# Performance work log

Measured on AMD Instinct MI355X. Metric: run time of the kernel, lower is better.

Reference implementation:

```python
import jax, jax.numpy as jnp
import numpy as np

B, T, I, H, NL, HORIZON, NQ = 256, 512, 64, 512, 2, 30, 3
MEDIAN_IDX = 1  # quantiles.index(0.5)


def _lstm_cell(xt, h, c, Wih, Whh, b):
    # PyTorch gate order: i, f, g, o
    g = xt @ Wih.T + h @ Whh.T + b
    i, f, gg, o = jnp.split(g, 4, axis=-1)
    c_new = jax.nn.sigmoid(f) * c + jax.nn.sigmoid(i) * jnp.tanh(gg)
    h_new = jax.nn.sigmoid(o) * jnp.tanh(c_new)
    return h_new, c_new


def _run_lstm_layer(xs, Wih, Whh, b):
    # xs: [T, B, in]; zero initial state (torch default)
    batch = xs.shape[1]
    hidden = Whh.shape[1]
    h0 = jnp.zeros((batch, hidden), xs.dtype)

    def step(carry, xt):
        h, c = carry
        h, c = _lstm_cell(xt, h, c, Wih, Whh, b)
        return (h, c), h

    (hT, cT), hs = jax.lax.scan(step, (h0, h0), xs)
    return hs, hT, cT


def setup_inputs() -> dict:
    key = jax.random.key(0)
    ks = jax.random.split(key, 24)
    k = 1.0 / np.sqrt(H)

    def u(kk, shape):
        return jax.random.uniform(kk, shape, jnp.float32, -k, k)

    inp = {
        "x": jax.random.normal(ks[0], (B, T, I), jnp.float32),
        # encoder layer 0 (input I) and layer 1 (input H)
        "enc_Wih0": u(ks[1], (4 * H, I)),
        "enc_Whh0": u(ks[2], (4 * H, H)),
        "enc_bih0": u(ks[3], (4 * H,)),
        "enc_bhh0": u(ks[4], (4 * H,)),
        "enc_Wih1": u(ks[5], (4 * H, H)),
        "enc_Whh1": u(ks[6], (4 * H, H)),
        "enc_bih1": u(ks[7], (4 * H,)),
        "enc_bhh1": u(ks[8], (4 * H,)),
        # decoder layer 0 (input H+1) and layer 1 (input H)
        "dec_Wih0": u(ks[9], (4 * H, H + 1)),
        "dec_Whh0": u(ks[10], (4 * H, H)),
        "dec_bih0": u(ks[11], (4 * H,)),
        "dec_bhh0": u(ks[12], (4 * H,)),
        "dec_Wih1": u(ks[13], (4 * H, H)),
        "dec_Whh1": u(ks[14], (4 * H, H)),
        "dec_bih1": u(ks[15], (4 * H,)),
        "dec_bhh1": u(ks[16], (4 * H,)),
        # attention: W [H,H] (no bias), V [H] (Linear(H,1) weight)
        "attn_W": u(ks[17], (H, H)),
        "attn_v": u(ks[18], (H,)),
        # output projection [NQ, H] + bias
        "out_W": u(ks[19], (NQ, H)),
        "out_b": u(ks[20], (NQ,)),
    }
    return inp


def reference(x, enc_Wih0, enc_Whh0, enc_bih0, enc_bhh0,
              enc_Wih1, enc_Whh1, enc_bih1, enc_bhh1,
              dec_Wih0, dec_Whh0, dec_bih0, dec_bhh0,
              dec_Wih1, dec_Whh1, dec_bih1, dec_bhh1,
              attn_W, attn_v, out_W, out_b):
    # ---- encoder: 2-layer LSTM over time (eval mode: no dropout) ----
    xs = jnp.transpose(x, (1, 0, 2))  # [T, B, I]
    hs0, _, _ = _run_lstm_layer(xs, enc_Wih0, enc_Whh0, enc_bih0 + enc_bhh0)
    hs1, h_last, c_last = _run_lstm_layer(hs0, enc_Wih1, enc_Whh1, enc_bih1 + enc_bhh1)
    encoder_outputs = jnp.transpose(hs1, (1, 0, 2))  # [B, T, H]

    # precompute W(encoder_outputs) once (same math as per-step recompute)
    enc_proj = jnp.einsum('bth,gh->btg', encoder_outputs, attn_W)  # [B, T, H]

    b_dec0 = dec_bih0 + dec_bhh0
    b_dec1 = dec_bih1 + dec_bhh1

    dec_input0 = x[:, -1, 0:1]  # [B, 1]

    def step(carry, _):
        h, c, inp = carry
        # Bahdanau attention
        dec_proj = h @ attn_W.T  # [B, H]
        energies = jnp.einsum('bth,h->bt', jnp.tanh(enc_proj + dec_proj[:, None, :]), attn_v)
        attn = jax.nn.softmax(energies, axis=1)  # [B, T]
        ctx = jnp.einsum('bt,bth->bh', attn, encoder_outputs)  # [B, H]
        # decoder LSTM, 1 timestep; both layers restart from the SAME (h, c)
        # (the module repeats the last layer's state across layers each step)
        x0 = jnp.concatenate([inp, ctx], axis=1)  # [B, H+1]
        h0, c0 = _lstm_cell(x0, h, c, dec_Wih0, dec_Whh0, b_dec0)
        h1, c1 = _lstm_cell(h0, h, c, dec_Wih1, dec_Whh1, b_dec1)
        out = h1 @ out_W.T + out_b  # [B, NQ]
        new_inp = out[:, MEDIAN_IDX:MEDIAN_IDX + 1]  # feed back median quantile
        return (h1, c1, new_inp), out

    _, preds = jax.lax.scan(step, (h_last, c_last, dec_input0), None, length=HORIZON)
    return jnp.transpose(preds, (1, 0, 2))  # [B, HORIZON, NQ]
```

## Files before the change

### kernel.cpp

```cpp
#include <hip/hip_runtime.h>


typedef _Float16 half_t;
typedef __attribute__((ext_vector_type(8)))  _Float16 f16x8;
typedef __attribute__((ext_vector_type(16))) float    f32x16;

#define MFMA(a,b,c) __builtin_amdgcn_mfma_f32_32x32x16_f16((a),(b),(c),0,0,0)
#define CBAR()      asm volatile("" ::: "memory")
#define AUXC 17

template<int N> __device__ __forceinline__ void waitvm() {
  asm volatile("s_waitcnt vmcnt(%0)" :: "n"(N) : "memory");
}

__device__ __forceinline__ float fsig(float x)  { return 1.0f / (1.0f + __expf(-x)); }
__device__ __forceinline__ float ftanh(float x) { return 1.0f - 2.0f / (1.0f + __expf(2.0f * x)); }

union FU { float f; unsigned u; };
union HU { _Float16 h; unsigned short u; };
__device__ __forceinline__ float ldfa(const float* p) {
  unsigned v = __hip_atomic_load((const unsigned*)p, __ATOMIC_RELAXED, __HIP_MEMORY_SCOPE_AGENT);
  FU c; c.u = v; return c.f;
}
__device__ __forceinline__ void stfa(float* p, float v) {
  FU c; c.f = v;
  __hip_atomic_store((unsigned*)p, c.u, __ATOMIC_RELAXED, __HIP_MEMORY_SCOPE_AGENT);
}
__device__ __forceinline__ void stha(half_t* p, float v) {
  HU c; c.h = (half_t)v;
  __hip_atomic_store((unsigned short*)p, c.u, __ATOMIC_RELAXED, __HIP_MEMORY_SCOPE_AGENT);
}
__device__ __forceinline__ void st64(float* p, float a, float b) {
  FU x, y; x.f = a; y.f = b;
  unsigned long long v = (unsigned long long)x.u | ((unsigned long long)y.u << 32);
  __hip_atomic_store((unsigned long long*)p, v, __ATOMIC_RELAXED, __HIP_MEMORY_SCOPE_AGENT);
}
__device__ __forceinline__ void ld64(const float* p, float& a, float& b) {
  unsigned long long v = __hip_atomic_load((const unsigned long long*)p, __ATOMIC_RELAXED, __HIP_MEMORY_SCOPE_AGENT);
  FU x, y; x.u = (unsigned)v; y.u = (unsigned)(v >> 32); a = x.f; b = y.f;
}

static constexpr size_t O_X16 = 0;
static constexpr size_t O_WL0 = O_X16 + (size_t)512*256*128*2;
static constexpr size_t O_WL1 = O_WL0 + (size_t)2048*640*2;
static constexpr size_t O_WP1 = O_WL1 + (size_t)2048*1024*2;
static constexpr size_t O_WD0 = O_WP1 + (size_t)4672*512*2;
static constexpr size_t O_WD1 = O_WD0 + (size_t)2048*512*2;
static constexpr size_t O_BL0 = O_WD1 + (size_t)2048*512*2;
static constexpr size_t O_BL1 = O_BL0 + 8192;
static constexpr size_t O_BD0 = O_BL1 + 8192;
static constexpr size_t O_BD1 = O_BD0 + 8192;
static constexpr size_t O_W0C = O_BD1 + 8192;
static constexpr size_t O_H0B = O_W0C + 8192;
static constexpr size_t O_H1B = O_H0B + (size_t)2*256*512*2;
static constexpr size_t O_HD1 = O_H1B + (size_t)2*256*512*2;
static constexpr size_t O_H0D = O_HD1 + (size_t)256*512*2;
static constexpr size_t O_CTX = O_H0D + (size_t)256*512*2;
static constexpr size_t O_C0  = O_CTX + (size_t)256*512*2;
static constexpr size_t O_C1  = O_C0  + (size_t)256*512*4;
static constexpr size_t O_INP = O_C1  + (size_t)256*512*4;
static constexpr size_t O_GAT = O_INP + 1024;
static constexpr size_t O_EO  = O_GAT + (size_t)256*4672*4;
static constexpr size_t O_EP  = O_EO  + (size_t)256*512*512*2;
static constexpr size_t WS_NEED = O_EP + (size_t)256*512*512*2;

__device__ __align__(4096) unsigned char g_ws[WS_NEED];
__device__ int g_bar[2048];

#define WSH(o) ((half_t*)(g_ws + (o)))
#define WSCH(o) ((const half_t*)(g_ws + (o)))
#define WSF(o) ((float*)(g_ws + (o)))
#define WSCF(o) ((const float*)(g_ws + (o)))
#define BLINE(i) (g_bar + ((size_t)(i) << 5))

__device__ __forceinline__ int gperm(int n) { return (n & 3) * 512 + (n >> 2); }

__device__ __forceinline__ void gbar_rel(int g, int sub) {
  __syncthreads();
  if (threadIdx.x == 0) {
    int* cnt = BLINE(g * 2 + sub);
    int* mst = BLINE(8 + g);
    int* gs  = BLINE(12 + g * 2 + sub);
    int old = __hip_atomic_load(gs, __ATOMIC_RELAXED, __HIP_MEMORY_SCOPE_AGENT);
    int a = __hip_atomic_fetch_add(cnt, 1, __ATOMIC_RELAXED, __HIP_MEMORY_SCOPE_AGENT);
    if (a == 31) {
      __hip_atomic_store(cnt, 0, __ATOMIC_RELAXED, __HIP_MEMORY_SCOPE_AGENT);
      int m = __hip_atomic_fetch_add(mst, 1, __ATOMIC_RELAXED, __HIP_MEMORY_SCOPE_AGENT);
      if (m == 1) {
        __hip_atomic_store(mst, 0, __ATOMIC_RELAXED, __HIP_MEMORY_SCOPE_AGENT);
        __hip_atomic_fetch_add(BLINE(12 + g * 2), 1, __ATOMIC_RELAXED, __HIP_MEMORY_SCOPE_AGENT);
        __hip_atomic_fetch_add(BLINE(12 + g * 2 + 1), 1, __ATOMIC_RELAXED, __HIP_MEMORY_SCOPE_AGENT);
      }
    }
    while (__hip_atomic_load(gs, __ATOMIC_RELAXED, __HIP_MEMORY_SCOPE_AGENT) == old)
      __builtin_amdgcn_s_sleep(2);
  }
  __syncthreads();
}

__device__ __forceinline__ void gbar_acq(int g, int sub) {
  __syncthreads();
  if (threadIdx.x == 0) {
    int* cnt = BLINE(g * 2 + sub);
    int* mst = BLINE(8 + g);
    int* gs  = BLINE(12 + g * 2 + sub);
    int old = __hip_atomic_load(gs, __ATOMIC_RELAXED, __HIP_MEMORY_SCOPE_AGENT);
    int a = __hip_atomic_fetch_add(cnt, 1, __ATOMIC_ACQ_REL, __HIP_MEMORY_SCOPE_AGENT);
    if (a == 31) {
      __hip_atomic_store(cnt, 0, __ATOMIC_RELAXED, __HIP_MEMORY_SCOPE_AGENT);
      int m = __hip_atomic_fetch_add(mst, 1, __ATOMIC_ACQ_REL, __HIP_MEMORY_SCOPE_AGENT);
      if (m == 1) {
        __hip_atomic_store(mst, 0, __ATOMIC_RELAXED, __HIP_MEMORY_SCOPE_AGENT);
        __hip_atomic_fetch_add(BLINE(12 + g * 2), 1, __ATOMIC_RELEASE, __HIP_MEMORY_SCOPE_AGENT);
        __hip_atomic_fetch_add(BLINE(12 + g * 2 + 1), 1, __ATOMIC_RELEASE, __HIP_MEMORY_SCOPE_AGENT);
      }
    }
    while (__hip_atomic_load(gs, __ATOMIC_RELAXED, __HIP_MEMORY_SCOPE_AGENT) == old)
      __builtin_amdgcn_s_sleep(2);
    (void)__hip_atomic_load(gs, __ATOMIC_ACQUIRE, __HIP_MEMORY_SCOPE_AGENT);
  }
  __syncthreads();
}

struct Seg { const half_t* p; int stride; int row0; };

template<int AXA, int AXB>
__device__ __forceinline__ void stageA(Seg sa, Seg sb, int cSplit, int c,
                                       int lane, int wid, char* dst) {
  bool isA = c < cSplit;
  Seg s = isA ? sa : sb;
  int kb = (isA ? c : (c - cSplit)) * 128;
  const half_t* g = s.p + (size_t)(s.row0 + (lane & 31)) * s.stride
                        + kb + (wid << 4) + ((lane >> 5) << 3);
  if (isA) {
    __builtin_amdgcn_global_load_lds(
        (const __attribute__((address_space(1))) unsigned int*)g,
        (__attribute__((address_space(3))) unsigned int*)dst, 16, 0, AXA);
    __builtin_amdgcn_global_load_lds(
        (const __attribute__((address_space(1))) unsigned int*)(g + (size_t)32 * s.stride),
        (__attribute__((address_space(3))) unsigned int*)(dst + 1024), 16, 0, AXA);
  } else {
    __builtin_amdgcn_global_load_lds(
        (const __attribute__((address_space(1))) unsigned int*)g,
        (__attribute__((address_space(3))) unsigned int*)dst, 16, 0, AXB);
    __builtin_amdgcn_global_load_lds(
        (const __attribute__((address_space(1))) unsigned int*)(g + (size_t)32 * s.stride),
        (__attribute__((address_space(3))) unsigned int*)(dst + 1024), 16, 0, AXB);
  }
}

template<int C, int NC, int CSPLIT, int AXA, int AXB>
__device__ __forceinline__ void kreg(Seg sa, Seg sb,
                                     const f16x8 (&B0)[8], const f16x8 (&B1)[8],
                                     int lane, int wid, char* asg, f32x16 acc[2][2]) {
  if constexpr (C < NC) {
    constexpr int rem = NC - 1 - C;
    waitvm<2 * (rem < 3 ? rem : 3)>();
    char* ab = asg + (size_t)(((C & 3) * 8 + wid)) * 2048 + lane * 16;
    f16x8 a0 = *(const f16x8*)ab;
    f16x8 a1 = *(const f16x8*)(ab + 1024);
    acc[0][0] = MFMA(a0, B0[C], acc[0][0]);
    acc[0][1] = MFMA(a0, B1[C], acc[0][1]);
    acc[1][0] = MFMA(a1, B0[C], acc[1][0]);
    acc[1][1] = MFMA(a1, B1[C], acc[1][1]);
    if constexpr (C + 4 < NC)
      stageA<AXA, AXB>(sa, sb, CSPLIT, C + 4, lane, wid,
                       asg + (size_t)((((C + 4) & 3) * 8 + wid)) * 2048);
    CBAR();
    kreg<C + 1, NC, CSPLIT, AXA, AXB>(sa, sb, B0, B1, lane, wid, asg, acc);
  }
}

template<int NC, int CSPLIT, int AXA, int AXB>
__device__ __forceinline__ void gemm_regB(Seg sa, Seg sb,
                                          const f16x8 (&B0)[8], const f16x8 (&B1)[8],
                                          int lane, int wid, char* asg, f32x16 acc[2][2]) {
  #pragma unroll
  for (int c = 0; c < (NC < 4 ? NC : 4); c++) {
    stageA<AXA, AXB>(sa, sb, CSPLIT, c, lane, wid, asg + (size_t)((c & 3) * 8 + wid) * 2048);
    CBAR();
  }
  kreg<0, NC, CSPLIT, AXA, AXB>(sa, sb, B0, B1, lane, wid, asg, acc);
}

template<int C, int NC>
__device__ __forceinline__ void kks(int lane, int wid, char* asg, f32x16 acc[2][2],
                                    f16x8 (&b0)[4], f16x8 (&b1)[4]) {
  if constexpr (C < NC) {
    waitvm<4 * (NC - 1 - C)>();
    char* ab = asg + (size_t)(C * 8 + wid) * 2048 + lane * 16;
    f16x8 a0 = *(const f16x8*)ab;
    f16x8 a1 = *(const f16x8*)(ab + 1024);
    acc[0][0] = MFMA(a0, b0[C], acc[0][0]);
    acc[0][1] = MFMA(a0, b1[C], acc[0][1]);
    acc[1][0] = MFMA(a1, b0[C], acc[1][0]);
    acc[1][1] = MFMA(a1, b1[C], acc[1][1]);
    CBAR();
    kks<C + 1, NC>(lane, wid, asg, acc, b0, b1);
  }
}

template<int NC, int AXA, int AXB>
__device__ __forceinline__ void gemm_ks(Seg sa, Seg sb, int cSplit, const half_t* Wt,
                                        int lane, int wid, char* asg, f32x16 acc[2][2]) {
  const half_t* wb = Wt + (wid << 1) * 512 + lane * 8;
  f16x8 b0[4], b1[4];
  #pragma unroll
  for (int c = 0; c < NC; c++) {
    stageA<AXA, AXB>(sa, sb, cSplit, c, lane, wid, asg + (size_t)(c * 8 + wid) * 2048);
    CBAR();
    b0[c] = *(const f16x8*)(wb + (size_t)c * 8192);
    b1[c] = *(const f16x8*)(wb + (size_t)c * 8192 + 512);
    CBAR();
  }
  kks<0, NC>(lane, wid, asg, acc, b0, b1);
}

__device__ __forceinline__ void acc_wr(float* dst, int lane, f32x16 acc[2][2]) {
  #pragma unroll
  for (int t = 0; t < 4; t++) {
    f32x16 a = acc[t >> 1][t & 1];
    #pragma unroll
    for (int r4 = 0; r4 < 4; r4++)
      *(float4*)(dst + ((t * 4 + r4) * 64 + lane) * 4) =
          make_float4(a[r4*4], a[r4*4+1], a[r4*4+2], a[r4*4+3]);
  }
}
__device__ __forceinline__ void acc_add(const float* src, int lane, f32x16 acc[2][2]) {
  #pragma unroll
  for (int t = 0; t < 4; t++) {
    #pragma unroll
    for (int r4 = 0; r4 < 4; r4++) {
      float4 v = *(const float4*)(src + ((t * 4 + r4) * 64 + lane) * 4);
      acc[t>>1][t&1][r4*4]   += v.x;
      acc[t>>1][t&1][r4*4+1] += v.y;
      acc[t>>1][t&1][r4*4+2] += v.z;
      acc[t>>1][t&1][r4*4+3] += v.w;
    }
  }
}
__device__ __forceinline__ void reduce4(f32x16 acc[2][2], float* red, int lane, int wid) {
  if (wid >= 4) acc_wr(red + (size_t)(wid - 4) * 4096, lane, acc);
  __syncthreads();
  if (wid < 4) {
    acc_add(red + (size_t)wid * 4096, lane, acc);
    acc_wr(red + (size_t)wid * 4096, lane, acc);
  }
  __syncthreads();
}
__device__ __forceinline__ int raddr(int row, int col) {
  int ms = row >> 5, rr = row & 31;
  int q = rr & 3, hl = (rr >> 2) & 1, r4 = rr >> 3;
  int ns = col >> 5;
  int lane = (hl << 5) | (col & 31);
  int t = ms * 2 + ns;
  return ((t * 4 + r4) * 64 + lane) * 4 + q;
}
__device__ __forceinline__ float red_sum(const float* red, int row, int col) {
  int i = raddr(row, col);
  return red[i] + red[4096 + i] + red[8192 + i] + red[12288 + i];
}

__global__ void __launch_bounds__(512, 2) kmain(const float* __restrict__ attn_v,
                                                const float* __restrict__ out_b,
                                                float* __restrict__ out) {
  __shared__ __align__(16) char asg[65536];
  __shared__ float red[16384];

  const half_t* x16 = WSCH(O_X16);
  const half_t* wL0 = WSCH(O_WL0);
  const half_t* wL1 = WSCH(O_WL1);
  const half_t* wP1 = WSCH(O_WP1);
  const half_t* wD0 = WSCH(O_WD0);
  const half_t* wD1 = WSCH(O_WD1);
  half_t* h0bB = WSH(O_H0B);
  half_t* h1bB = WSH(O_H1B);
  half_t* hd1  = WSH(O_HD1);
  half_t* h0d  = WSH(O_H0D);
  half_t* ctx  = WSH(O_CTX);
  half_t* eo   = WSH(O_EO);
  half_t* ep   = WSH(O_EP);
  float* c1 = WSF(O_C1);
  float* inp = WSF(O_INP);
  float* gates = WSF(O_GAT);

  const int tid = threadIdx.x;
  const int wid = tid >> 6;
  const int lane = tid & 63;
  const int g = blockIdx.x & 3;
  const int r = blockIdx.x >> 2;
  const int sub = r & 1;
  const int m0 = g << 6;
  const f32x16 zv = {0,0,0,0,0,0,0,0,0,0,0,0,0,0,0,0};

  {
    const bool isL1 = r >= 32;
    const int n0 = (r & 31) << 6;

    const half_t* wbase = isL1 ? (wL1 + (size_t)(n0 >> 6) * (8 * 8192))
                               : (wL0 + (size_t)(n0 >> 6) * (5 * 8192));
    const half_t* wb = wbase + (wid << 1) * 512 + lane * 8;
    const int ncB = isL1 ? 8 : 5;
    f16x8 B0[8], B1[8];
    #pragma unroll
    for (int c = 0; c < 8; c++) {
      if (c < ncB) {
        B0[c] = *(const f16x8*)(wb + (size_t)c * 8192);
        B1[c] = *(const f16x8*)(wb + (size_t)c * 8192 + 512);
      }
    }
    const int eu = tid & 15;
    const int ebl = tid >> 4;
    const float* bias = isL1 ? WSCF(O_BL1) : WSCF(O_BL0);
    float4 breg = *(const float4*)&bias[n0 + eu * 4];
    float creg0 = 0.f, creg1 = 0.f;

    for (int s = 0; s <= 512; s++) {
      const bool active = isL1 ? (s > 0) : (s < 512);
      if (active) {
        const half_t* h0r = h0bB + (size_t)((s + 1) & 1) * (256 * 512);
        f32x16 acc[2][2] = {{zv, zv}, {zv, zv}};
        int t;
        if (!isL1) {
          t = s;
          gemm_regB<5, 1, 0, AUXC>(Seg{x16, 128, t * 256 + m0}, Seg{h0r, 512, m0},
                                   B0, B1, lane, wid, asg, acc);
        } else {
          t = s - 1;
          const half_t* h1r = h1bB + (size_t)(s & 1) * (256 * 512);
          gemm_regB<8, 4, AUXC, AUXC>(Seg{h0r, 512, m0}, Seg{h1r, 512, m0},
                                      B0, B1, lane, wid, asg, acc);
        }
        reduce4(acc, red, lane, wid);
        half_t* hb = isL1 ? (h1bB + (size_t)((s - 1) & 1) * (256 * 512))
                          : (h0bB + (size_t)(s & 1) * (256 * 512));
        #pragma unroll
        for (int it = 0; it < 2; it++) {
          int bl = ebl + it * 32;
          float gi = red_sum(red, bl, eu * 4 + 0) + breg.x;
          float gf = red_sum(red, bl, eu * 4 + 1) + breg.y;
          float gz = red_sum(red, bl, eu * 4 + 2) + breg.z;
          float go = red_sum(red, bl, eu * 4 + 3) + breg.w;
          float cold = it ? creg1 : creg0;
          float cn = fsig(gf) * cold + fsig(gi) * ftanh(gz);
          float hn = fsig(go) * ftanh(cn);
          if (it) creg1 = cn; else creg0 = cn;
          int bg = m0 + bl, ug = (n0 >> 2) + eu;
          stha(&hb[bg * 512 + ug], hn);
          if (isL1) eo[((size_t)bg * 512 + t) * 512 + ug] = (half_t)hn;
        }
      }
      gbar_rel(g, sub);
    }

    if (isL1) {
      int ug = (n0 >> 2) + eu;
      c1[(m0 + ebl) * 512 + ug] = creg0;
      c1[(m0 + ebl + 32) * 512 + ug] = creg1;
    }
  }
  gbar_acq(g, sub);

  for (int j = 0; j < 64; j++) {
    const int jj = r * 64 + j;
    const int ml = jj >> 3;
    const int nt = jj & 7;
    const int row0 = (g << 15) + ml * 64;
    f32x16 acc[2][2] = {{zv, zv}, {zv, zv}};
    gemm_ks<4, 0, 0>(Seg{eo, 512, row0}, Seg{eo, 512, row0}, 4,
                     wP1 + (size_t)nt * (4 * 8192), lane, wid, asg, acc);
    reduce4(acc, red, lane, wid);
    {
      int row = tid >> 3, col = (tid & 7) * 8;
      f16x8 h8;
      #pragma unroll
      for (int q = 0; q < 8; q++) h8[q] = (half_t)red_sum(red, row, col + q);
      *(f16x8*)&ep[(size_t)(row0 + row) * 512 + nt * 64 + col] = h8;
    }
    __syncthreads();
  }
  gbar_acq(g, sub);

  for (int d = 0; d <= 30; d++) {
    const half_t* hs = (d == 0) ? (h1bB + 256 * 512) : hd1;
    for (int jj = r; jj < 73; jj += 64) {
      const int n0p = jj * 64;
      f32x16 acc[2][2] = {{zv, zv}, {zv, zv}};
      gemm_ks<4, AUXC, AUXC>(Seg{hs, 512, m0}, Seg{hs, 512, m0}, 4,
                             wP1 + (size_t)jj * (4 * 8192), lane, wid, asg, acc);
      reduce4(acc, red, lane, wid);
      if (n0p < 4608) {
        #pragma unroll
        for (int it = 0; it < 2; it++) {
          int q = it * 512 + tid;
          int row = q >> 4, col = (q & 15) * 4;
          float v0 = red_sum(red, row, col + 0);
          float v1 = red_sum(red, row, col + 1);
          float v2 = red_sum(red, row, col + 2);
          float v3 = red_sum(red, row, col + 3);
          float* dst = &gates[(size_t)(m0 + row) * 4672 + n0p + col];
          st64(dst, v0, v1);
          st64(dst + 2, v2, v3);
        }
      } else if (d > 0) {
        if (tid < 64) {
          int bg = m0 + tid;
          float v0 = red_sum(red, tid, 0) + out_b[0];
          float v1 = red_sum(red, tid, 1) + out_b[1];
          float v2 = red_sum(red, tid, 2) + out_b[2];
          out[(size_t)bg * 90 + (d - 1) * 3 + 0] = v0;
          out[(size_t)bg * 90 + (d - 1) * 3 + 1] = v1;
          out[(size_t)bg * 90 + (d - 1) * 3 + 2] = v2;
          stfa(&inp[bg], v1);
        }
      }
      __syncthreads();
    }
    gbar_rel(g, sub);
    if (d == 30) break;

    {
      const int b = m0 + r;
      float* dpb = red;
      float* vb  = red + 512;
      float* eb  = red + 1024;
      float* ab2 = red + 2048;
      float* sc  = red + 2560;
      float* pm  = red + 4096;
      dpb[tid] = ldfa(&gates[(size_t)b * 4672 + tid]);
      vb[tid]  = attn_v[tid];
      __syncthreads();
      const half_t* eprow = ep + ((size_t)b << 18) + (size_t)(wid * 64) * 512 + lane * 8;
      for (int tt = 0; tt < 64; tt++) {
        f16x8 e8 = *(const f16x8*)(eprow + (size_t)tt * 512);
        float sum = 0.f;
        #pragma unroll
        for (int jq = 0; jq < 8; jq++)
          sum += vb[lane * 8 + jq] * ftanh((float)e8[jq] + dpb[lane * 8 + jq]);
        #pragma unroll
        for (int off = 32; off > 0; off >>= 1) sum += __shfl_down(sum, off, 64);
        if (lane == 0) eb[wid * 64 + tt] = sum;
      }
      __syncthreads();
      float e0 = eb[tid];
      float mx = e0;
      #pragma unroll
      for (int off = 32; off > 0; off >>= 1) mx = fmaxf(mx, __shfl_xor(mx, off, 64));
      if (lane == 0) sc[wid] = mx;
      __syncthreads();
      mx = sc[0];
      #pragma unroll
      for (int q = 1; q < 8; q++) mx = fmaxf(mx, sc[q]);
      float x0 = __expf(e0 - mx);
      float ssum = x0;
      #pragma unroll
      for (int off = 32; off > 0; off >>= 1) ssum += __shfl_xor(ssum, off, 64);
      __syncthreads();
      if (lane == 0) sc[8 + wid] = ssum;
      __syncthreads();
      float tot = sc[8];
      #pragma unroll
      for (int q = 1; q < 8; q++) tot += sc[8 + q];
      float inv = 1.f / tot;
      ab2[tid] = x0 * inv;
      __syncthreads();
      float pacc[8] = {0,0,0,0,0,0,0,0};
      const half_t* eow = eo + ((size_t)b << 18) + (size_t)(wid * 64) * 512 + lane * 8;
      for (int tt = 0; tt < 64; tt++) {
        f16x8 h8 = *(const f16x8*)(eow + (size_t)tt * 512);
        float at = ab2[wid * 64 + tt];
        #pragma unroll
        for (int jq = 0; jq < 8; jq++) pacc[jq] += at * (float)h8[jq];
      }
      #pragma unroll
      for (int jq = 0; jq < 8; jq++) pm[wid * 512 + lane * 8 + jq] = pacc[jq];
      __syncthreads();
      float sctx = 0.f;
      #pragma unroll
      for (int w = 0; w < 8; w++) sctx += pm[w * 512 + tid];
      stha(&ctx[(b << 9) + tid], sctx);
    }
    gbar_rel(g, sub);

    if (r < 32) {
      const int n0 = r << 6;
      f32x16 acc[2][2] = {{zv, zv}, {zv, zv}};
      gemm_ks<4, AUXC, AUXC>(Seg{ctx, 512, m0}, Seg{ctx, 512, m0}, 4,
                             wD0 + (size_t)(n0 >> 6) * (4 * 8192), lane, wid, asg, acc);
      reduce4(acc, red, lane, wid);
      const float* bD0 = WSCF(O_BD0);
      const float* w0c = WSCF(O_W0C);
      #pragma unroll
      for (int it = 0; it < 2; it++) {
        int q = it * 512 + tid;
        int u = q & 15, bl = q >> 4;
        int bg = m0 + bl, ug = (n0 >> 2) + u, nl = n0 + u * 4;
        float p0, p1, p2, p3;
        ld64(&gates[(size_t)bg * 4672 + 512 + nl], p0, p1);
        ld64(&gates[(size_t)bg * 4672 + 512 + nl + 2], p2, p3);
        float4 b4 = *(const float4*)&bD0[nl];
        float4 w4 = *(const float4*)&w0c[nl];
        float iv = ldfa(&inp[bg]);
        float gi = red_sum(red, bl, u*4+0) + p0 + b4.x + iv * w4.x;
        float gf = red_sum(red, bl, u*4+1) + p1 + b4.y + iv * w4.y;
        float gz = red_sum(red, bl, u*4+2) + p2 + b4.z + iv * w4.z;
        float go = red_sum(red, bl, u*4+3) + p3 + b4.w + iv * w4.w;
        float cold = c1[bg * 512 + ug];
        float cn = fsig(gf) * cold + fsig(gi) * ftanh(gz);
        stha(&h0d[bg * 512 + ug], fsig(go) * ftanh(cn));
      }
    }
    gbar_rel(g, sub);

    if (r < 32) {
      const int n0 = r << 6;
      f32x16 acc[2][2] = {{zv, zv}, {zv, zv}};
      gemm_ks<4, AUXC, AUXC>(Seg{h0d, 512, m0}, Seg{h0d, 512, m0}, 4,
                             wD1 + (size_t)(n0 >> 6) * (4 * 8192), lane, wid, asg, acc);
      reduce4(acc, red, lane, wid);
      const float* bD1 = WSCF(O_BD1);
      #pragma unroll
      for (int it = 0; it < 2; it++) {
        int q = it * 512 + tid;
        int u = q & 15, bl = q >> 4;
        int bg = m0 + bl, ug = (n0 >> 2) + u, nl = n0 + u * 4;
        float p0, p1, p2, p3;
        ld64(&gates[(size_t)bg * 4672 + 2560 + nl], p0, p1);
        ld64(&gates[(size_t)bg * 4672 + 2560 + nl + 2], p2, p3);
        float4 b4 = *(const float4*)&bD1[nl];
        float gi = red_sum(red, bl, u*4+0) + p0 + b4.x;
        float gf = red_sum(red, bl, u*4+1) + p1 + b4.y;
        float gz = red_sum(red, bl, u*4+2) + p2 + b4.z;
        float go = red_sum(red, bl, u*4+3) + p3 + b4.w;
        float cold = c1[bg * 512 + ug];
        float cn = fsig(gf) * cold + fsig(gi) * ftanh(gz);
        float hn = fsig(go) * ftanh(cn);
        c1[bg * 512 + ug] = cn;
        stha(&hd1[bg * 512 + ug], hn);
      }
    }
    gbar_rel(g, sub);
  }
}

__global__ void kpackB(size_t dstOff, int id, int Ntiles, int NC,
                       const float* s0, const float* s1,
                       const float* s2, const float* s3) {
  half_t* dst = (half_t*)(g_ws + dstOff);
  size_t total = (size_t)Ntiles * NC * 8192;
  size_t i = (size_t)blockIdx.x * 256 + threadIdx.x;
  size_t stride = (size_t)gridDim.x * 256;
  for (size_t e = i; e < total; e += stride) {
    int j = e & 7;
    int l = (e >> 3) & 63;
    int bh = (e >> 9) & 1;
    int w = (e >> 10) & 7;
    int tc = (int)(e >> 13);
    int c = tc % NC;
    int tile = tc / NC;
    int n = tile * 64 + bh * 32 + (l & 31);
    int k = c * 128 + w * 16 + ((l >> 5) << 3) + j;
    float v = 0.f;
    if (id == 0) {
      int pn = gperm(n);
      if (k < 64) v = s0[(size_t)pn * 64 + k];
      else if (k >= 128) v = s1[(size_t)pn * 512 + (k - 128)];
    } else if (id == 1) {
      int pn = gperm(n);
      v = (k < 512) ? s0[(size_t)pn * 512 + k] : s1[(size_t)pn * 512 + (k - 512)];
    } else if (id == 2) {
      if (n < 512) v = s0[((size_t)n << 9) + k];
      else if (n < 2560) v = s1[((size_t)gperm(n - 512) << 9) + k];
      else if (n < 4608) v = s2[((size_t)gperm(n - 2560) << 9) + k];
      else if (n < 4611) v = s3[((size_t)(n - 4608) << 9) + k];
    } else if (id == 3) {
      v = s0[(size_t)gperm(n) * 513 + 1 + k];
    } else {
      v = s0[((size_t)gperm(n) << 9) + k];
    }
    dst[e] = (half_t)v;
  }
}

__global__ void kmisc(const float* ebih0, const float* ebhh0, const float* ebih1, const float* ebhh1,
                      const float* dbih0, const float* dbhh0, const float* dbih1, const float* dbhh1,
                      const float* dWih0, const float* x) {
  float* bL0 = WSF(O_BL0);
  float* bL1 = WSF(O_BL1);
  float* bD0 = WSF(O_BD0);
  float* bD1 = WSF(O_BD1);
  float* w0c = WSF(O_W0C);
  half_t* h0b = WSH(O_H0B);
  half_t* h1b = WSH(O_H1B);
  float* c1 = WSF(O_C1);
  float* inp = WSF(O_INP);
  int i = blockIdx.x * 256 + threadIdx.x, stride = gridDim.x * 256;
  for (int idx = i; idx < 262144; idx += stride) {
    if (idx < 2048) {
      int pn = gperm(idx);
      bL0[idx] = ebih0[pn] + ebhh0[pn];
      bL1[idx] = ebih1[pn] + ebhh1[pn];
      bD0[idx] = dbih0[pn] + dbhh0[pn];
      bD1[idx] = dbih1[pn] + dbhh1[pn];
      w0c[idx] = dWih0[(size_t)pn * 513];
      g_bar[idx] = 0;
    }
    if (idx < 256) inp[idx] = x[((size_t)idx * 512 + 511) * 64];
    h0b[idx] = (half_t)0.f;
    h1b[idx] = (half_t)0.f;
    if (idx < 131072) c1[idx] = 0.f;
  }
}

__global__ void kx16(const float* x) {
  half_t* dst = WSH(O_X16);
  size_t i = (size_t)blockIdx.x * 256 + threadIdx.x;
  size_t stride = (size_t)gridDim.x * 256;
  for (size_t e = i; e < (size_t)512 * 256 * 128; e += stride) {
    int t = (int)(e >> 15);
    int b = (int)((e >> 7) & 255);
    int ii = (int)(e & 127);
    dst[e] = (ii < 64) ? (half_t)x[((size_t)b * 512 + t) * 64 + ii] : (half_t)0.f;
  }
}

extern "C" void kernel_launch(void* const* d_in, const int* in_sizes, int n_in,
                              void* d_out, int out_size, void* d_ws, size_t ws_size,
                              hipStream_t stream) {
  const float* x     = (const float*)d_in[0];
  const float* eWih0 = (const float*)d_in[1];
  const float* eWhh0 = (const float*)d_in[2];
  const float* ebih0 = (const float*)d_in[3];
  const float* ebhh0 = (const float*)d_in[4];
  const float* eWih1 = (const float*)d_in[5];
  const float* eWhh1 = (const float*)d_in[6];
  const float* ebih1 = (const float*)d_in[7];
  const float* ebhh1 = (const float*)d_in[8];
  const float* dWih0 = (const float*)d_in[9];
  const float* dWhh0 = (const float*)d_in[10];
  const float* dbih0 = (const float*)d_in[11];
  const float* dbhh0 = (const float*)d_in[12];
  const float* dWih1 = (const float*)d_in[13];
  const float* dWhh1 = (const float*)d_in[14];
  const float* dbih1 = (const float*)d_in[15];
  const float* dbhh1 = (const float*)d_in[16];
  const float* attnW = (const float*)d_in[17];
  const float* attnv = (const float*)d_in[18];
  const float* outW  = (const float*)d_in[19];
  const float* outb  = (const float*)d_in[20];
  (void)in_sizes; (void)n_in; (void)out_size; (void)d_ws; (void)ws_size;

  kpackB<<<1024, 256, 0, stream>>>(O_WL0, 0, 32, 5, eWih0, eWhh0, nullptr, nullptr);
  kpackB<<<1024, 256, 0, stream>>>(O_WL1, 1, 32, 8, eWih1, eWhh1, nullptr, nullptr);
  kpackB<<<1024, 256, 0, stream>>>(O_WP1, 2, 73, 4, attnW, dWhh0, dWhh1, outW);
  kpackB<<<1024, 256, 0, stream>>>(O_WD0, 3, 32, 4, dWih0, nullptr, nullptr, nullptr);
  kpackB<<<1024, 256, 0, stream>>>(O_WD1, 4, 32, 4, dWih1, nullptr, nullptr, nullptr);
  kmisc<<<1024, 256, 0, stream>>>(ebih0, ebhh0, ebih1, ebhh1,
                                  dbih0, dbhh0, dbih1, dbhh1, dWih0, x);
  kx16<<<2048, 256, 0, stream>>>(x);

  float* outp = (float*)d_out;
  void* args[] = {(void*)&attnv, (void*)&outb, (void*)&outp};
  hipError_t e = hipLaunchCooperativeKernel((void*)kmain, dim3(256), dim3(512),
                                            args, 0, stream);
  if (e != hipSuccess) {
    kmain<<<dim3(256), dim3(512), 0, stream>>>(attnv, outb, outp);
  }
}
```

Baseline: 8.505 ms.

## Replace counter group barrier with per-block flag barrier and tree reduce

```diff
diff --git a/kernel.cpp b/kernel.cpp
--- a/kernel.cpp
+++ b/kernel.cpp
@@ -66,6 +66,7 @@
 
 __device__ __align__(4096) unsigned char g_ws[WS_NEED];
 __device__ int g_bar[2048];
+__device__ int g_flags[1024];
 
 #define WSH(o) ((half_t*)(g_ws + (o)))
 #define WSCH(o) ((const half_t*)(g_ws + (o)))
@@ -75,25 +76,18 @@
 
 __device__ __forceinline__ int gperm(int n) { return (n & 3) * 512 + (n >> 2); }
 
-__device__ __forceinline__ void gbar_rel(int g, int sub) {
+__device__ __forceinline__ void gbarf(int g, int r, int step) {
   __syncthreads();
-  if (threadIdx.x == 0) {
-    int* cnt = BLINE(g * 2 + sub);
-    int* mst = BLINE(8 + g);
-    int* gs  = BLINE(12 + g * 2 + sub);
-    int old = __hip_atomic_load(gs, __ATOMIC_RELAXED, __HIP_MEMORY_SCOPE_AGENT);
-    int a = __hip_atomic_fetch_add(cnt, 1, __ATOMIC_RELAXED, __HIP_MEMORY_SCOPE_AGENT);
-    if (a == 31) {
-      __hip_atomic_store(cnt, 0, __ATOMIC_RELAXED, __HIP_MEMORY_SCOPE_AGENT);
-      int m = __hip_atomic_fetch_add(mst, 1, __ATOMIC_RELAXED, __HIP_MEMORY_SCOPE_AGENT);
-      if (m == 1) {
-        __hip_atomic_store(mst, 0, __ATOMIC_RELAXED, __HIP_MEMORY_SCOPE_AGENT);
-        __hip_atomic_fetch_add(BLINE(12 + g * 2), 1, __ATOMIC_RELAXED, __HIP_MEMORY_SCOPE_AGENT);
-        __hip_atomic_fetch_add(BLINE(12 + g * 2 + 1), 1, __ATOMIC_RELAXED, __HIP_MEMORY_SCOPE_AGENT);
-      }
-    }
-    while (__hip_atomic_load(gs, __ATOMIC_RELAXED, __HIP_MEMORY_SCOPE_AGENT) == old)
-      __builtin_amdgcn_s_sleep(2);
+  if (threadIdx.x < 64) {
+    if (threadIdx.x == 0)
+      __hip_atomic_store(&g_flags[(g << 6) + r], step,
+                         __ATOMIC_RELAXED, __HIP_MEMORY_SCOPE_AGENT);
+    const int* fp = &g_flags[(g << 6) + threadIdx.x];
+    for (;;) {
+      int v = __hip_atomic_load(fp, __ATOMIC_RELAXED, __HIP_MEMORY_SCOPE_AGENT);
+      if (__all(v >= step)) break;
+      __builtin_amdgcn_s_sleep(1);
+    }
   }
   __syncthreads();
 }
@@ -239,26 +233,31 @@
     }
   }
 }
-__device__ __forceinline__ void reduce4(f32x16 acc[2][2], float* red, int lane, int wid) {
+__device__ __forceinline__ void reduce8(f32x16 acc[2][2], float* red, int lane, int wid) {
   if (wid >= 4) acc_wr(red + (size_t)(wid - 4) * 4096, lane, acc);
   __syncthreads();
-  if (wid < 4) {
-    acc_add(red + (size_t)wid * 4096, lane, acc);
-    acc_wr(red + (size_t)wid * 4096, lane, acc);
-  }
+  if (wid < 4) acc_add(red + (size_t)wid * 4096, lane, acc);
+  if (wid == 2 || wid == 3) acc_wr(red + (size_t)wid * 4096, lane, acc);
   __syncthreads();
-}
-__device__ __forceinline__ int raddr(int row, int col) {
-  int ms = row >> 5, rr = row & 31;
-  int q = rr & 3, hl = (rr >> 2) & 1, r4 = rr >> 3;
-  int ns = col >> 5;
-  int lane = (hl << 5) | (col & 31);
-  int t = ms * 2 + ns;
-  return ((t * 4 + r4) * 64 + lane) * 4 + q;
-}
-__device__ __forceinline__ float red_sum(const float* red, int row, int col) {
-  int i = raddr(row, col);
-  return red[i] + red[4096 + i] + red[8192 + i] + red[12288 + i];
+  if (wid < 2) {
+    acc_add(red + (size_t)(wid + 2) * 4096, lane, acc);
+    float* zone = red + 8192 + (size_t)wid * 4096;
+    #pragma unroll
+    for (int ms = 0; ms < 2; ms++)
+      #pragma unroll
+      for (int ns = 0; ns < 2; ns++)
+        #pragma unroll
+        for (int rr = 0; rr < 16; rr++) {
+          int row = ms * 32 + (rr & 3) + ((rr >> 2) << 3) + ((lane >> 5) << 2);
+          zone[row * 64 + ns * 32 + (lane & 31)] = acc[ms][ns][rr];
+        }
+  }
+  __syncthreads();
+}
+__device__ __forceinline__ float4 rsum4(const float* red, int row, int col) {
+  float4 a = *(const float4*)&red[8192 + row * 64 + col];
+  float4 b = *(const float4*)&red[12288 + row * 64 + col];
+  return make_float4(a.x + b.x, a.y + b.y, a.z + b.z, a.w + b.w);
 }
 
 __global__ void __launch_bounds__(512, 2) kmain(const float* __restrict__ attn_v,
@@ -292,6 +291,7 @@
   const int sub = r & 1;
   const int m0 = g << 6;
   const f32x16 zv = {0,0,0,0,0,0,0,0,0,0,0,0,0,0,0,0};
+  int bstep = 0;
 
   {
     const bool isL1 = r >= 32;
@@ -331,16 +331,15 @@
           gemm_regB<8, 4, AUXC, AUXC>(Seg{h0r, 512, m0}, Seg{h1r, 512, m0},
                                       B0, B1, lane, wid, asg, acc);
         }
-        reduce4(acc, red, lane, wid);
+        reduce8(acc, red, lane, wid);
         half_t* hb = isL1 ? (h1bB + (size_t)((s - 1) & 1) * (256 * 512))
                           : (h0bB + (size_t)(s & 1) * (256 * 512));
         #pragma unroll
         for (int it = 0; it < 2; it++) {
           int bl = ebl + it * 32;
-          float gi = red_sum(red, bl, eu * 4 + 0) + breg.x;
-          float gf = red_sum(red, bl, eu * 4 + 1) + breg.y;
-          float gz = red_sum(red, bl, eu * 4 + 2) + breg.z;
-          float go = red_sum(red, bl, eu * 4 + 3) + breg.w;
+          float4 g4 = rsum4(red, bl, eu * 4);
+          float gi = g4.x + breg.x, gf = g4.y + breg.y;
+          float gz = g4.z + breg.z, go = g4.w + breg.w;
           float cold = it ? creg1 : creg0;
           float cn = fsig(gf) * cold + fsig(gi) * ftanh(gz);
           float hn = fsig(go) * ftanh(cn);
@@ -350,7 +349,7 @@
           if (isL1) eo[((size_t)bg * 512 + t) * 512 + ug] = (half_t)hn;
         }
       }
-      gbar_rel(g, sub);
+      gbarf(g, r, ++bstep);
     }
 
     if (isL1) {
@@ -369,12 +368,14 @@
     f32x16 acc[2][2] = {{zv, zv}, {zv, zv}};
     gemm_ks<4, 0, 0>(Seg{eo, 512, row0}, Seg{eo, 512, row0}, 4,
                      wP1 + (size_t)nt * (4 * 8192), lane, wid, asg, acc);
-    reduce4(acc, red, lane, wid);
+    reduce8(acc, red, lane, wid);
     {
       int row = tid >> 3, col = (tid & 7) * 8;
+      float4 a0 = rsum4(red, row, col);
+      float4 a1 = rsum4(red, row, col + 4);
       f16x8 h8;
-      #pragma unroll
-      for (int q = 0; q < 8; q++) h8[q] = (half_t)red_sum(red, row, col + q);
+      h8[0] = (half_t)a0.x; h8[1] = (half_t)a0.y; h8[2] = (half_t)a0.z; h8[3] = (half_t)a0.w;
+      h8[4] = (half_t)a1.x; h8[5] = (half_t)a1.y; h8[6] = (half_t)a1.z; h8[7] = (half_t)a1.w;
       *(f16x8*)&ep[(size_t)(row0 + row) * 512 + nt * 64 + col] = h8;
     }
     __syncthreads();
@@ -388,26 +389,23 @@
       f32x16 acc[2][2] = {{zv, zv}, {zv, zv}};
       gemm_ks<4, AUXC, AUXC>(Seg{hs, 512, m0}, Seg{hs, 512, m0}, 4,
                              wP1 + (size_t)jj * (4 * 8192), lane, wid, asg, acc);
-      reduce4(acc, red, lane, wid);
+      reduce8(acc, red, lane, wid);
       if (n0p < 4608) {
         #pragma unroll
         for (int it = 0; it < 2; it++) {
           int q = it * 512 + tid;
           int row = q >> 4, col = (q & 15) * 4;
-          float v0 = red_sum(red, row, col + 0);
-          float v1 = red_sum(red, row, col + 1);
-          float v2 = red_sum(red, row, col + 2);
-          float v3 = red_sum(red, row, col + 3);
+          float4 v4 = rsum4(red, row, col);
           float* dst = &gates[(size_t)(m0 + row) * 4672 + n0p + col];
-          st64(dst, v0, v1);
-          st64(dst + 2, v2, v3);
+          st64(dst, v4.x, v4.y);
+          st64(dst + 2, v4.z, v4.w);
         }
       } else if (d > 0) {
         if (tid < 64) {
           int bg = m0 + tid;
-          float v0 = red_sum(red, tid, 0) + out_b[0];
-          float v1 = red_sum(red, tid, 1) + out_b[1];
-          float v2 = red_sum(red, tid, 2) + out_b[2];
+          float v0 = red[8192 + tid * 64 + 0] + red[12288 + tid * 64 + 0] + out_b[0];
+          float v1 = red[8192 + tid * 64 + 1] + red[12288 + tid * 64 + 1] + out_b[1];
+          float v2 = red[8192 + tid * 64 + 2] + red[12288 + tid * 64 + 2] + out_b[2];
           out[(size_t)bg * 90 + (d - 1) * 3 + 0] = v0;
           out[(size_t)bg * 90 + (d - 1) * 3 + 1] = v1;
           out[(size_t)bg * 90 + (d - 1) * 3 + 2] = v2;
@@ -416,7 +414,7 @@
       }
       __syncthreads();
     }
-    gbar_rel(g, sub);
+    gbarf(g, r, ++bstep);
     if (d == 30) break;
 
     {
@@ -430,13 +428,24 @@
       dpb[tid] = ldfa(&gates[(size_t)b * 4672 + tid]);
       vb[tid]  = attn_v[tid];
       __syncthreads();
+      float va[8], da[8];
+      {
+        float4 t0 = *(const float4*)&vb[lane * 8];
+        float4 t1 = *(const float4*)&vb[lane * 8 + 4];
+        float4 t2 = *(const float4*)&dpb[lane * 8];
+        float4 t3 = *(const float4*)&dpb[lane * 8 + 4];
+        va[0]=t0.x; va[1]=t0.y; va[2]=t0.z; va[3]=t0.w;
+        va[4]=t1.x; va[5]=t1.y; va[6]=t1.z; va[7]=t1.w;
+        da[0]=t2.x; da[1]=t2.y; da[2]=t2.z; da[3]=t2.w;
+        da[4]=t3.x; da[5]=t3.y; da[6]=t3.z; da[7]=t3.w;
+      }
       const half_t* eprow = ep + ((size_t)b << 18) + (size_t)(wid * 64) * 512 + lane * 8;
       for (int tt = 0; tt < 64; tt++) {
         f16x8 e8 = *(const f16x8*)(eprow + (size_t)tt * 512);
         float sum = 0.f;
         #pragma unroll
         for (int jq = 0; jq < 8; jq++)
-          sum += vb[lane * 8 + jq] * ftanh((float)e8[jq] + dpb[lane * 8 + jq]);
+          sum += va[jq] * ftanh((float)e8[jq] + da[jq]);
         #pragma unroll
         for (int off = 32; off > 0; off >>= 1) sum += __shfl_down(sum, off, 64);
         if (lane == 0) eb[wid * 64 + tt] = sum;
@@ -480,14 +489,14 @@
       for (int w = 0; w < 8; w++) sctx += pm[w * 512 + tid];
       stha(&ctx[(b << 9) + tid], sctx);
     }
-    gbar_rel(g, sub);
+    gbarf(g, r, ++bstep);
 
     if (r < 32) {
       const int n0 = r << 6;
       f32x16 acc[2][2] = {{zv, zv}, {zv, zv}};
       gemm_ks<4, AUXC, AUXC>(Seg{ctx, 512, m0}, Seg{ctx, 512, m0}, 4,
                              wD0 + (size_t)(n0 >> 6) * (4 * 8192), lane, wid, asg, acc);
-      reduce4(acc, red, lane, wid);
+      reduce8(acc, red, lane, wid);
       const float* bD0 = WSCF(O_BD0);
       const float* w0c = WSCF(O_W0C);
       #pragma unroll
@@ -495,43 +504,45 @@
         int q = it * 512 + tid;
         int u = q & 15, bl = q >> 4;
         int bg = m0 + bl, ug = (n0 >> 2) + u, nl = n0 + u * 4;
+        float4 g4 = rsum4(red, bl, u * 4);
         float p0, p1, p2, p3;
         ld64(&gates[(size_t)bg * 4672 + 512 + nl], p0, p1);
         ld64(&gates[(size_t)bg * 4672 + 512 + nl + 2], p2, p3);
         float4 b4 = *(const float4*)&bD0[nl];
         float4 w4 = *(const float4*)&w0c[nl];
         float iv = ldfa(&inp[bg]);
-        float gi = red_sum(red, bl, u*4+0) + p0 + b4.x + iv * w4.x;
-        float gf = red_sum(red, bl, u*4+1) + p1 + b4.y + iv * w4.y;
-        float gz = red_sum(red, bl, u*4+2) + p2 + b4.z + iv * w4.z;
-        float go = red_sum(red, bl, u*4+3) + p3 + b4.w + iv * w4.w;
+        float gi = g4.x + p0 + b4.x + iv * w4.x;
+        float gf = g4.y + p1 + b4.y + iv * w4.y;
+        float gz = g4.z + p2 + b4.z + iv * w4.z;
+        float go = g4.w + p3 + b4.w + iv * w4.w;
         float cold = c1[bg * 512 + ug];
         float cn = fsig(gf) * cold + fsig(gi) * ftanh(gz);
         stha(&h0d[bg * 512 + ug], fsig(go) * ftanh(cn));
       }
     }
-    gbar_rel(g, sub);
+    gbarf(g, r, ++bstep);
 
     if (r < 32) {
       const int n0 = r << 6;
       f32x16 acc[2][2] = {{zv, zv}, {zv, zv}};
       gemm_ks<4, AUXC, AUXC>(Seg{h0d, 512, m0}, Seg{h0d, 512, m0}, 4,
                              wD1 + (size_t)(n0 >> 6) * (4 * 8192), lane, wid, asg, acc);
-      reduce4(acc, red, lane, wid);
+      reduce8(acc, red, lane, wid);
       const float* bD1 = WSCF(O_BD1);
       #pragma unroll
       for (int it = 0; it < 2; it++) {
         int q = it * 512 + tid;
         int u = q & 15, bl = q >> 4;
         int bg = m0 + bl, ug = (n0 >> 2) + u, nl = n0 + u * 4;
+        float4 g4 = rsum4(red, bl, u * 4);
         float p0, p1, p2, p3;
         ld64(&gates[(size_t)bg * 4672 + 2560 + nl], p0, p1);
         ld64(&gates[(size_t)bg * 4672 + 2560 + nl + 2], p2, p3);
         float4 b4 = *(const float4*)&bD1[nl];
-        float gi = red_sum(red, bl, u*4+0) + p0 + b4.x;
-        float gf = red_sum(red, bl, u*4+1) + p1 + b4.y;
-        float gz = red_sum(red, bl, u*4+2) + p2 + b4.z;
-        float go = red_sum(red, bl, u*4+3) + p3 + b4.w;
+        float gi = g4.x + p0 + b4.x;
+        float gf = g4.y + p1 + b4.y;
+        float gz = g4.z + p2 + b4.z;
+        float go = g4.w + p3 + b4.w;
         float cold = c1[bg * 512 + ug];
         float cn = fsig(gf) * cold + fsig(gi) * ftanh(gz);
         float hn = fsig(go) * ftanh(cn);
@@ -539,7 +550,7 @@
         stha(&hd1[bg * 512 + ug], hn);
       }
     }
-    gbar_rel(g, sub);
+    gbarf(g, r, ++bstep);
   }
 }
 
@@ -605,6 +616,7 @@
       w0c[idx] = dWih0[(size_t)pn * 513];
       g_bar[idx] = 0;
     }
+    if (idx < 1024) g_flags[idx] = 0;
     if (idx < 256) inp[idx] = x[((size_t)idx * 512 + 511) * 64];
     h0b[idx] = (half_t)0.f;
     h1b[idx] = (half_t)0.f;
```

Measured after the change: 8.495 ms. No clear change (-0.1%).
